# Optimization experiments

Measured on AMD Instinct MI355X. Metric: run time of the kernel, lower is better.

## Reference

```python
import jax, jax.numpy as jnp
import numpy as np

DIM = 192
HEADS = 6

def conv1x1(x, w):
    # x: [b,c,h,w], w: [out,in]
    return jnp.einsum('oi,bihw->bohw', w, x)

def dwconv3x3(x, w):
    # x: [b,c,h,w], w: [c,1,3,3] depthwise
    return jax.lax.conv_general_dilated(
        x, w, window_strides=(1, 1), padding='SAME',
        dimension_numbers=('NCHW', 'OIHW', 'NCHW'),
        feature_group_count=x.shape[1])

def l2norm(x, eps=1e-12):
    n = jnp.sqrt(jnp.sum(x * x, axis=-1, keepdims=True))
    return x / jnp.maximum(n, eps)

def setup_inputs() -> dict:
    key = jax.random.key(0)
    ks = jax.random.split(key, 9)
    b, c, h, w = 8, DIM, 128, 128
    s = 1.0 / np.sqrt(c)
    return {
        'x': jax.random.normal(ks[0], (b, c, h, w), jnp.float32),
        'Wq': jax.random.normal(ks[1], (c, c), jnp.float32) * s,
        'Wk': jax.random.normal(ks[2], (c, c), jnp.float32) * s,
        'Wv': jax.random.normal(ks[3], (c, c), jnp.float32) * s,
        'Wq_dw': jax.random.normal(ks[4], (c, 1, 3, 3), jnp.float32) * (1.0 / 3.0),
        'Wk_dw': jax.random.normal(ks[5], (c, 1, 3, 3), jnp.float32) * (1.0 / 3.0),
        'Wv_dw': jax.random.normal(ks[6], (c, 1, 3, 3), jnp.float32) * (1.0 / 3.0),
        'rescale': jnp.ones((HEADS, 1, 1), jnp.float32),
        'Wp': jax.random.normal(ks[7], (c, c), jnp.float32) * s,
    }

def reference(x, Wq, Wk, Wv, Wq_dw, Wk_dw, Wv_dw, rescale, Wp):
    b, c, h, w = x.shape
    hd = c // HEADS  # per-head channels
    q = dwconv3x3(conv1x1(x, Wq), Wq_dw).reshape(b, HEADS, hd, h * w)
    k = dwconv3x3(conv1x1(x, Wk), Wk_dw).reshape(b, HEADS, hd, h * w)
    v = dwconv3x3(conv1x1(x, Wv), Wv_dw).reshape(b, HEADS, hd, h * w)
    q = l2norm(q)
    k = l2norm(k)
    # attn: [b, heads, hd, hd] -- small channel-wise attention
    attn = jnp.einsum('bhcn,bhdn->bhcd', q, k) * rescale
    attn = jax.nn.softmax(attn, axis=-1)
    out = jnp.einsum('bhcd,bhdn->bhcn', attn, v).reshape(b, c, h, w)
    return conv1x1(out, Wp)
```

## Files before the change

### kernel.cpp

```cpp
#include <hip/hip_runtime.h>
#include <hip/hip_bf16.h>


using bf16x8 = __attribute__((ext_vector_type(8))) short;
using f32x4  = __attribute__((ext_vector_type(4))) float;
using fvec4  = __attribute__((ext_vector_type(4))) float;

#define NB     8
#define CDIM   192
#define NHEADS 6
#define IMGW   128
#define NPIX   16384

__device__ __forceinline__ float b2f(unsigned short u){
  return __uint_as_float(((unsigned int)u) << 16);
}
__device__ __forceinline__ unsigned short f2b(float f){
  unsigned int x = __float_as_uint(f);
  return (unsigned short)((x + 0x7FFFu + ((x >> 16) & 1u)) >> 16);
}
__device__ __forceinline__ float ldT(const void* p, size_t i, int isbf){
  return isbf ? b2f(((const unsigned short*)p)[i]) : ((const float*)p)[i];
}
__device__ __forceinline__ f32x4 MF(bf16x8 a, bf16x8 b, f32x4 c){
  return __builtin_amdgcn_mfma_f32_16x16x32_bf16(a, b, c, 0, 0, 0);
}

__global__ void k_detect(const unsigned short* x, int* flag){
  int l = threadIdx.x;
  int cnt = 0;
#pragma unroll
  for (int i = 0; i < 2; ++i){
    unsigned short u = x[(l*2 + i)*2];
    float a = fabsf(b2f(u));
    if (a == 0.f || (a > 1e-4f && a < 20.f)) ++cnt;
  }
  int tot = __popcll(__ballot(cnt >= 1)) + __popcll(__ballot(cnt >= 2));
  if (l == 0) *flag = (tot > 64) ? 1 : 0;
}

__global__ __launch_bounds__(256) void k_prep(const void* Wq, const void* Wk, const void* Wv,
    unsigned short* Wqkv, const int* flag){
  int i = blockIdx.x*256 + threadIdx.x;
  if (i >= 576*192) return;
  int isbf = *flag;
  int m = i / 192, kk = i % 192;
  int t = m / 192;
  const void* W = (t == 0) ? Wq : (t == 1) ? Wk : Wv;
  Wqkv[i] = f2b(ldT(W, (size_t)(m % 192)*192 + kk, isbf));
}

__global__ __launch_bounds__(256) void k_conv1(const void* x, const unsigned short* Wqkv,
    unsigned short* q0, unsigned short* k0, unsigned short* v0, const int* flag){
  __shared__ unsigned short Bt[64][200];
  __shared__ unsigned short outb[192][72];
  int tid = threadIdx.x;
  int ntr = blockIdx.x, b = blockIdx.y;
  int nt = (ntr & 7)*32 + (ntr >> 3);
  int n0 = nt * 64;
  int isbf = *flag;
  if (isbf){
    const unsigned short* xs = (const unsigned short*)x;
    for (int r = tid; r < 1536; r += 256){
      int k = r >> 3, j8 = (r & 7) * 8;
      int s = (r & 7) << 3;
      bf16x8 v = *(const bf16x8*)(xs + (size_t)(b*CDIM + k)*NPIX + n0 + j8);
      int kx = k ^ s;
#pragma unroll
      for (int i = 0; i < 8; ++i) Bt[j8+i][kx] = (unsigned short)v[i];
    }
  } else {
    const float* xf = (const float*)x;
    for (int r = tid; r < 3072; r += 256){
      int k = r >> 4, j4 = (r & 15) * 4;
      int s = ((j4 >> 3) & 7) << 3;
      fvec4 v = *(const fvec4*)(xf + (size_t)(b*CDIM + k)*NPIX + n0 + j4);
      int kx = k ^ s;
#pragma unroll
      for (int i = 0; i < 4; ++i) Bt[j4+i][kx] = f2b(v[i]);
    }
  }
  __syncthreads();
  int w = tid >> 6, l = tid & 63, lr = l & 15, lk = l >> 4;
#pragma unroll 1
  for (int t = 0; t < 3; ++t){
    f32x4 acc[3][4] = {};
    for (int kc = 0; kc < 6; ++kc){
      bf16x8 af[3];
#pragma unroll
      for (int g = 0; g < 3; ++g)
        af[g] = *(const bf16x8*)(Wqkv + ((size_t)t*CDIM + g*64 + w*16 + lr)*CDIM + kc*32 + lk*8);
#pragma unroll
      for (int nf = 0; nf < 4; ++nf){
        int nrow = nf*16 + lr;
        int s = ((nrow >> 3) & 7) << 3;
        bf16x8 bfv = *(const bf16x8*)(&Bt[nrow][(kc*32 + lk*8) ^ s]);
#pragma unroll
        for (int g = 0; g < 3; ++g) acc[g][nf] = MF(af[g], bfv, acc[g][nf]);
      }
    }
    __syncthreads();
#pragma unroll
    for (int g = 0; g < 3; ++g)
#pragma unroll
      for (int nf = 0; nf < 4; ++nf)
#pragma unroll
        for (int r = 0; r < 4; ++r)
          outb[g*64 + w*16 + lk*4 + r][nf*16 + lr] = f2b(acc[g][nf][r]);
    __syncthreads();
    unsigned short* dst = ((t == 0) ? q0 : (t == 1) ? k0 : v0) + (size_t)b*CDIM*NPIX;
    for (int e = tid; e < 1536; e += 256){
      int m = e >> 3, p8 = (e & 7) * 8;
      *(bf16x8*)(dst + (size_t)m*NPIX + n0 + p8) = *(const bf16x8*)(&outb[m][p8]);
    }
  }
}

__global__ __launch_bounds__(256) void k_dw(unsigned short* q0, unsigned short* k0,
    unsigned short* v0, const void* wqd, const void* wkd, const void* wvd,
    float* Nsq, const int* flag){
  __shared__ unsigned short img[128][136];
  __shared__ unsigned short outb[128][136];
  __shared__ float wred[4];
  int tid = threadIdx.x;
  int t = blockIdx.x, c = blockIdx.y, b = blockIdx.z;
  int isbf = *flag;
  unsigned short* base = ((t == 0) ? q0 : (t == 1) ? k0 : v0) + (size_t)(b*CDIM + c)*NPIX;
  const void* wd = (t == 0) ? wqd : (t == 1) ? wkd : wvd;
  float w9[9];
#pragma unroll
  for (int e = 0; e < 9; ++e) w9[e] = ldT(wd, (size_t)c*9 + e, isbf);
  for (int r = tid; r < 2048; r += 256){
    int row = r >> 4, col8 = (r & 15)*8;
    *(bf16x8*)(&img[row][col8]) = *(const bf16x8*)(base + row*IMGW + col8);
  }
  __syncthreads();
  int tr = tid >> 2, tc = tid & 3;
  int c0 = tc * 32, r0 = tr * 2;
  const bf16x8 zv = {0,0,0,0,0,0,0,0};
  int  rowi[4]; bool valid[4];
  bf16x8 cur[4], nxt[4];
  float carry[4];
#pragma unroll
  for (int d = 0; d < 4; ++d){
    rowi[d] = r0 - 1 + d;
    valid[d] = (rowi[d] >= 0) && (rowi[d] < 128);
    cur[d] = valid[d] ? *(const bf16x8*)(&img[rowi[d]][c0]) : zv;
    carry[d] = (valid[d] && c0 > 0) ? b2f(img[rowi[d]][c0 - 1]) : 0.f;
  }
  float sq = 0.f;
#pragma unroll
  for (int j = 0; j < 4; ++j){
    float right0[4];
    if (j < 3){
#pragma unroll
      for (int d = 0; d < 4; ++d){
        nxt[d] = valid[d] ? *(const bf16x8*)(&img[rowi[d]][c0 + 8*(j+1)]) : zv;
        right0[d] = b2f((unsigned short)nxt[d][0]);
      }
    } else {
#pragma unroll
      for (int d = 0; d < 4; ++d)
        right0[d] = (valid[d] && (c0 + 32 < 128)) ? b2f(img[rowi[d]][c0 + 32]) : 0.f;
    }
    float f[4][8];
#pragma unroll
    for (int d = 0; d < 4; ++d)
#pragma unroll
      for (int i = 0; i < 8; ++i) f[d][i] = b2f((unsigned short)cur[d][i]);
#pragma unroll
    for (int rr = 0; rr < 2; ++rr){
      float o[8];
#pragma unroll
      for (int cc = 0; cc < 8; ++cc){
        float a = 0.f;
#pragma unroll
        for (int d2 = 0; d2 < 3; ++d2){
          int d = rr + d2;
          float lf = (cc == 0) ? carry[d] : f[d][cc-1];
          float md = f[d][cc];
          float rt = (cc == 7) ? right0[d] : f[d][cc+1];
          a = fmaf(w9[d2*3+0], lf, a);
          a = fmaf(w9[d2*3+1], md, a);
          a = fmaf(w9[d2*3+2], rt, a);
        }
        o[cc] = a;
        if (t < 2) sq = fmaf(a, a, sq);
      }
      bf16x8 ov;
#pragma unroll
      for (int cc = 0; cc < 8; ++cc) ov[cc] = (short)f2b(o[cc]);
      *(bf16x8*)(&outb[r0 + rr][c0 + 8*j]) = ov;
    }
#pragma unroll
    for (int d = 0; d < 4; ++d) carry[d] = f[d][7];
    if (j < 3){
#pragma unroll
      for (int d = 0; d < 4; ++d) cur[d] = nxt[d];
    }
  }
  if (t < 2){
#pragma unroll
    for (int off = 32; off > 0; off >>= 1) sq += __shfl_xor(sq, off);
    if ((tid & 63) == 0) wred[tid >> 6] = sq;
  }
  __syncthreads();
  for (int e = tid; e < 2048; e += 256){
    int row = e >> 4, p8 = (e & 15) * 8;
    *(bf16x8*)(base + row*IMGW + p8) = *(const bf16x8*)(&outb[row][p8]);
  }
  if (t < 2 && tid == 0)
    Nsq[((size_t)b*2 + t)*CDIM + c] = wred[0] + wred[1] + wred[2] + wred[3];
}

__global__ __launch_bounds__(256) void k_gram(const unsigned short* qd,
    const unsigned short* kd, float* Spart){
  __shared__ float S_lds[1024];
  int tid = threadIdx.x;
  int cs = blockIdx.x, h = blockIdx.y, b = blockIdx.z;
  int w = tid >> 6, l = tid & 63, lr = l & 15, lk = l >> 4;
  for (int e = tid; e < 1024; e += 256) S_lds[e] = 0.f;
  __syncthreads();
  const unsigned short* qb = qd + (size_t)(b*CDIM + h*32)*NPIX;
  const unsigned short* kb = kd + (size_t)(b*CDIM + h*32)*NPIX;
  f32x4 g4[2][2] = {};
  int pxb = cs*2048 + w*512 + lk*8;
#pragma unroll
  for (int kc = 0; kc < 16; ++kc){
    int px = pxb + kc*32;
    bf16x8 a0 = *(const bf16x8*)(qb + (size_t)lr*NPIX + px);
    bf16x8 a1 = *(const bf16x8*)(qb + (size_t)(16+lr)*NPIX + px);
    bf16x8 b0 = *(const bf16x8*)(kb + (size_t)lr*NPIX + px);
    bf16x8 b1 = *(const bf16x8*)(kb + (size_t)(16+lr)*NPIX + px);
    g4[0][0] = MF(a0, b0, g4[0][0]);
    g4[0][1] = MF(a0, b1, g4[0][1]);
    g4[1][0] = MF(a1, b0, g4[1][0]);
    g4[1][1] = MF(a1, b1, g4[1][1]);
  }
  for (int wv = 0; wv < 4; ++wv){
    if (w == wv){
#pragma unroll
      for (int mi = 0; mi < 2; ++mi)
#pragma unroll
        for (int ni = 0; ni < 2; ++ni)
#pragma unroll
          for (int r = 0; r < 4; ++r)
            S_lds[(mi*16 + lk*4 + r)*32 + ni*16 + lr] += g4[mi][ni][r];
    }
    __syncthreads();
  }
  int bidx = (b*NHEADS + h)*8 + cs;
  for (int e = tid; e < 1024; e += 256) Spart[(size_t)bidx*1024 + e] = S_lds[e];
}

__global__ __launch_bounds__(256) void k_attn(const float* Spart, const float* Nsq,
    const void* rescale, float* attnG, const int* flag){
  __shared__ float S[1024];
  __shared__ float rn[64];
  int bh = blockIdx.x, tid = threadIdx.x;
  int b = bh / NHEADS, h = bh % NHEADS;
  int isbf = *flag;
  for (int e = tid; e < 1024; e += 256){
    float a = 0.f;
    for (int st = 0; st < 8; ++st) a += Spart[((size_t)bh*8 + st)*1024 + e];
    S[e] = a;
  }
  if (tid < 64){
    int t = tid >> 5, ch = h*32 + (tid & 31);
    float a = Nsq[((size_t)b*2 + t)*CDIM + ch];
    rn[tid] = 1.f / fmaxf(sqrtf(a), 1e-12f);
  }
  __syncthreads();
  if (tid < 32){
    float sc = ldT(rescale, h, isbf);
    float lo[32], mx = -1e30f;
#pragma unroll
    for (int d = 0; d < 32; ++d){
      lo[d] = S[tid*32 + d] * rn[tid] * rn[32 + d] * sc;
      mx = fmaxf(mx, lo[d]);
    }
    float sum = 0.f;
#pragma unroll
    for (int d = 0; d < 32; ++d){ lo[d] = __expf(lo[d] - mx); sum += lo[d]; }
    float inv = 1.f / sum;
#pragma unroll
    for (int d = 0; d < 32; ++d) attnG[(size_t)bh*1024 + tid*32 + d] = lo[d] * inv;
  }
}

__global__ __launch_bounds__(256) void k_mmat(const void* Wp, const float* attnG,
    unsigned short* Mb, const int* flag){
  __shared__ float at[NHEADS*1024];
  __shared__ float wp[32][200];
  int b = blockIdx.x, og = blockIdx.y, tid = threadIdx.x;
  int isbf = *flag;
  for (int e = tid; e < NHEADS*1024; e += 256) at[e] = attnG[(size_t)b*NHEADS*1024 + e];
  for (int e = tid; e < 32*192; e += 256){
    int r = e / 192, cdx = e % 192;
    wp[r][cdx] = ldT(Wp, (size_t)(og*32 + r)*CDIM + cdx, isbf);
  }
  __syncthreads();
  int r = tid >> 3, cg = tid & 7;
#pragma unroll 1
  for (int i = 0; i < 24; ++i){
    int dg = cg*24 + i;
    int hh = dg >> 5, d = dg & 31;
    float a = 0.f;
#pragma unroll
    for (int cc = 0; cc < 32; ++cc)
      a += wp[r][hh*32 + cc] * at[hh*1024 + cc*32 + d];
    Mb[(size_t)b*CDIM*CDIM + (size_t)(og*32 + r)*CDIM + dg] = f2b(a);
  }
}

__global__ __launch_bounds__(256) void k_out(const unsigned short* v, const unsigned short* Mb,
    void* out, const int* flag){
  __shared__ unsigned short Bt[64][200];
  __shared__ unsigned short outb[192][72];
  int tid = threadIdx.x;
  int ntr = blockIdx.x, b = blockIdx.y;
  int nt = (ntr & 7)*32 + (ntr >> 3);
  int n0 = nt * 64;
  for (int r = tid; r < 1536; r += 256){
    int k = r >> 3, j8 = (r & 7) * 8;
    int s = (r & 7) << 3;
    bf16x8 vv = *(const bf16x8*)(v + (size_t)(b*CDIM + k)*NPIX + n0 + j8);
    int kx = k ^ s;
#pragma unroll
    for (int i = 0; i < 8; ++i) Bt[j8+i][kx] = (unsigned short)vv[i];
  }
  __syncthreads();
  int w = tid >> 6, l = tid & 63, lr = l & 15, lk = l >> 4;
  const unsigned short* A = Mb + (size_t)b*CDIM*CDIM;
  f32x4 acc[3][4] = {};
  for (int kc = 0; kc < 6; ++kc){
    bf16x8 af[3];
#pragma unroll
    for (int g = 0; g < 3; ++g)
      af[g] = *(const bf16x8*)(A + (size_t)(g*64 + w*16 + lr)*CDIM + kc*32 + lk*8);
#pragma unroll
    for (int nf = 0; nf < 4; ++nf){
      int nrow = nf*16 + lr;
      int s = ((nrow >> 3) & 7) << 3;
      bf16x8 bfv = *(const bf16x8*)(&Bt[nrow][(kc*32 + lk*8) ^ s]);
#pragma unroll
      for (int g = 0; g < 3; ++g) acc[g][nf] = MF(af[g], bfv, acc[g][nf]);
    }
  }
  int isbf = *flag;
  if (isbf){
#pragma unroll
    for (int g = 0; g < 3; ++g)
#pragma unroll
      for (int nf = 0; nf < 4; ++nf)
#pragma unroll
        for (int r = 0; r < 4; ++r)
          outb[g*64 + w*16 + lk*4 + r][nf*16 + lr] = f2b(acc[g][nf][r]);
    __syncthreads();
    unsigned short* dst = (unsigned short*)out + (size_t)b*CDIM*NPIX;
    for (int e = tid; e < 1536; e += 256){
      int m = e >> 3, p8 = (e & 7) * 8;
      *(bf16x8*)(dst + (size_t)m*NPIX + n0 + p8) = *(const bf16x8*)(&outb[m][p8]);
    }
  } else {
#pragma unroll
    for (int g = 0; g < 3; ++g)
#pragma unroll
      for (int nf = 0; nf < 4; ++nf)
#pragma unroll
        for (int r = 0; r < 4; ++r){
          int m = g*64 + w*16 + lk*4 + r;
          ((float*)out)[(size_t)(b*CDIM + m)*NPIX + n0 + nf*16 + lr] = acc[g][nf][r];
        }
  }
}

extern "C" void kernel_launch(void* const* d_in, const int* in_sizes, int n_in,
                              void* d_out, int out_size, void* d_ws, size_t ws_size,
                              hipStream_t stream){
  const void* x   = d_in[0];
  const void* Wq  = d_in[1];
  const void* Wk  = d_in[2];
  const void* Wv  = d_in[3];
  const void* Wqd = d_in[4];
  const void* Wkd = d_in[5];
  const void* Wvd = d_in[6];
  const void* rsc = d_in[7];
  const void* Wp  = d_in[8];

  char* ws = (char*)d_ws;
  size_t o = 0;
  int* flag             = (int*)(ws + o);            o += 256;
  unsigned short* Wqkv  = (unsigned short*)(ws + o); o += (size_t)576*192*2;
  unsigned short* q0    = (unsigned short*)(ws + o); o += (size_t)NB*CDIM*NPIX*2;
  unsigned short* k0    = (unsigned short*)(ws + o); o += (size_t)NB*CDIM*NPIX*2;
  unsigned short* v0    = (unsigned short*)(ws + o); o += (size_t)NB*CDIM*NPIX*2;
  float* Spart          = (float*)(ws + o);          o += (size_t)384*1024*4;
  float* Nsq            = (float*)(ws + o);          o += (size_t)NB*2*CDIM*4;
  float* attnG          = (float*)(ws + o);          o += (size_t)48*1024*4;
  unsigned short* Mb    = (unsigned short*)(ws + o); o += (size_t)NB*CDIM*CDIM*2;

  k_detect<<<dim3(1), 64, 0, stream>>>((const unsigned short*)x, flag);
  k_prep  <<<dim3(432), 256, 0, stream>>>(Wq, Wk, Wv, Wqkv, flag);
  k_conv1 <<<dim3(256, NB), 256, 0, stream>>>(x, Wqkv, q0, k0, v0, flag);
  k_dw    <<<dim3(3, CDIM, NB), 256, 0, stream>>>(q0, k0, v0, Wqd, Wkd, Wvd, Nsq, flag);
  k_gram  <<<dim3(8, NHEADS, NB), 256, 0, stream>>>(q0, k0, Spart);
  k_attn  <<<dim3(48), 256, 0, stream>>>(Spart, Nsq, rsc, attnG, flag);
  k_mmat  <<<dim3(NB, 6), 256, 0, stream>>>(Wp, attnG, Mb, flag);
  k_out   <<<dim3(256, NB), 256, 0, stream>>>(v0, Mb, d_out, flag);
}
```

Before: 260.7 us.

## Fuse depthwise conv with Gram computation and store conv1 output in tiled layout

Merges the depthwise 3x3 conv and the q·k Gram kernel into one kernel. Each block processes 8 image rows for one head, keeps the convolved q and k rows in LDS, and computes partial Gram and norm sums there, so the q/k round trip through global memory goes away. Conv1 output is now written in a per-64-pixel tile layout [b][tile][c][64], and the convolved v goes to a separate buffer in the same layout that k_out reads. The cost is heavy LDS use (about 160KB, one block per CU), row-by-row syncs, and twice as many partial sums to reduce in k_attn.

```diff
diff --git a/kernel.cpp b/kernel.cpp
--- a/kernel.cpp
+++ b/kernel.cpp
@@ -11,6 +11,7 @@
 #define NHEADS 6
 #define IMGW   128
 #define NPIX   16384
+#define DDP    1032
 
 __device__ __forceinline__ float b2f(unsigned short u){
   return __uint_as_float(((unsigned int)u) << 16);
@@ -108,130 +109,122 @@
         for (int r = 0; r < 4; ++r)
           outb[g*64 + w*16 + lk*4 + r][nf*16 + lr] = f2b(acc[g][nf][r]);
     __syncthreads();
-    unsigned short* dst = ((t == 0) ? q0 : (t == 1) ? k0 : v0) + (size_t)b*CDIM*NPIX;
+    unsigned short* dstT = ((t == 0) ? q0 : (t == 1) ? k0 : v0)
+                         + (size_t)(b*256 + nt)*CDIM*64;
     for (int e = tid; e < 1536; e += 256){
       int m = e >> 3, p8 = (e & 7) * 8;
-      *(bf16x8*)(dst + (size_t)m*NPIX + n0 + p8) = *(const bf16x8*)(&outb[m][p8]);
-    }
-  }
-}
-
-__global__ __launch_bounds__(256) void k_dw(unsigned short* q0, unsigned short* k0,
-    unsigned short* v0, const void* wqd, const void* wkd, const void* wvd,
-    float* Nsq, const int* flag){
-  __shared__ unsigned short img[128][136];
-  __shared__ unsigned short outb[128][136];
-  __shared__ float wred[4];
+      *(bf16x8*)(dstT + m*64 + p8) = *(const bf16x8*)(&outb[m][p8]);
+    }
+  }
+}
+
+__global__ __launch_bounds__(256, 1) void k_dwg(const unsigned short* q0,
+    const unsigned short* k0, const unsigned short* v0,
+    const void* wqd, const void* wkd, const void* wvd,
+    unsigned short* v1, float* Spart, float* Npart, const int* flag){
+  __shared__ unsigned short ring[3][32][136];
+  __shared__ unsigned short qd[32*DDP];
+  __shared__ unsigned short kd[32*DDP];
+  __shared__ float S_lds[1024];
+  __shared__ float nbuf[2][32];
   int tid = threadIdx.x;
-  int t = blockIdx.x, c = blockIdx.y, b = blockIdx.z;
-  int isbf = *flag;
-  unsigned short* base = ((t == 0) ? q0 : (t == 1) ? k0 : v0) + (size_t)(b*CDIM + c)*NPIX;
-  const void* wd = (t == 0) ? wqd : (t == 1) ? wkd : wvd;
-  float w9[9];
-#pragma unroll
-  for (int e = 0; e < 9; ++e) w9[e] = ldT(wd, (size_t)c*9 + e, isbf);
-  for (int r = tid; r < 2048; r += 256){
-    int row = r >> 4, col8 = (r & 15)*8;
-    *(bf16x8*)(&img[row][col8]) = *(const bf16x8*)(base + row*IMGW + col8);
+  int s = blockIdx.x, h = blockIdx.y, b = blockIdx.z;
+  int isbf = *flag;
+  int r0 = s*8;
+  for (int e = tid; e < 1024; e += 256) S_lds[e] = 0.f;
+  int ch = tid >> 3, p0 = (tid & 7) * 16;
+  int chg = h*32 + ch;
+  int sch0 = tid >> 4,      sseg0 = tid & 15;
+  int sch1 = (tid+256) >> 4, sseg1 = (tid+256) & 15;
+  const int order[3] = {2, 0, 1};
+#pragma unroll 1
+  for (int tt = 0; tt < 3; ++tt){
+    int t = order[tt];
+    const unsigned short* src = (t == 0) ? q0 : (t == 1) ? k0 : v0;
+    const void* wd = (t == 0) ? wqd : (t == 1) ? wkd : wvd;
+    unsigned short* dd = (t == 1) ? kd : qd;
+    float w9[9];
+#pragma unroll
+    for (int e = 0; e < 9; ++e) w9[e] = ldT(wd, (size_t)chg*9 + e, isbf);
+    const bf16x8 zv = {0,0,0,0,0,0,0,0};
+    auto gload = [&](int r, bf16x8& a, bf16x8& c){
+      if (r >= 0 && r < 128){
+        int t0 = 2*r + (sseg0 >> 3), t1 = 2*r + (sseg1 >> 3);
+        a = *(const bf16x8*)(src + ((size_t)(b*256 + t0)*CDIM + h*32 + sch0)*64 + (sseg0 & 7)*8);
+        c = *(const bf16x8*)(src + ((size_t)(b*256 + t1)*CDIM + h*32 + sch1)*64 + (sseg1 & 7)*8);
+      } else { a = zv; c = zv; }
+    };
+    auto dswr = [&](int r, bf16x8 a, bf16x8 c){
+      int sl = ((r % 3) + 3) % 3;
+      *(bf16x8*)(&ring[sl][sch0][sseg0*8]) = a;
+      *(bf16x8*)(&ring[sl][sch1][sseg1*8]) = c;
+    };
+    bf16x8 pa, pc;
+    gload(r0-1, pa, pc); dswr(r0-1, pa, pc);
+    gload(r0,   pa, pc); dswr(r0,   pa, pc);
+    gload(r0+1, pa, pc);
+    __syncthreads();
+    float sq = 0.f;
+#pragma unroll 1
+    for (int rr = 0; rr < 8; ++rr){
+      int r = r0 + rr;
+      dswr(r+1, pa, pc);
+      __syncthreads();
+      if (rr < 7) gload(r+2, pa, pc);
+      float f[3][18];
+#pragma unroll
+      for (int j = 0; j < 3; ++j){
+        int sl = (((r-1+j) % 3) + 3) % 3;
+        const unsigned short* rp = &ring[sl][ch][0];
+        bf16x8 m0 = *(const bf16x8*)(rp + p0);
+        bf16x8 m1 = *(const bf16x8*)(rp + p0 + 8);
+        f[j][0]  = (p0 > 0)   ? b2f(rp[p0-1])  : 0.f;
+        f[j][17] = (p0 < 112) ? b2f(rp[p0+16]) : 0.f;
+#pragma unroll
+        for (int i = 0; i < 8; ++i){ f[j][1+i] = b2f((unsigned short)m0[i]);
+                                     f[j][9+i] = b2f((unsigned short)m1[i]); }
+      }
+      bf16x8 o0, o1;
+#pragma unroll
+      for (int c = 0; c < 16; ++c){
+        float a = 0.f;
+#pragma unroll
+        for (int j = 0; j < 3; ++j)
+#pragma unroll
+          for (int d = 0; d < 3; ++d)
+            a = fmaf(w9[j*3+d], f[j][c+d], a);
+        if (t < 2) sq = fmaf(a, a, sq);
+        if (c < 8) o0[c] = (short)f2b(a); else o1[c-8] = (short)f2b(a);
+      }
+      *(bf16x8*)(&dd[ch*DDP + rr*128 + p0])     = o0;
+      *(bf16x8*)(&dd[ch*DDP + rr*128 + p0 + 8]) = o1;
+      __syncthreads();
+    }
+    if (t < 2){
+      sq += __shfl_xor(sq, 1); sq += __shfl_xor(sq, 2); sq += __shfl_xor(sq, 4);
+      if ((tid & 7) == 0) nbuf[t][ch] = sq;
+    } else {
+      __syncthreads();
+      for (int e = tid; e < 4096; e += 256){
+        int c = e >> 7, chunk = e & 127;
+        int rr2 = chunk >> 4, px = (chunk & 15) * 8;
+        int tile = 2*(r0 + rr2) + (px >> 6);
+        *(bf16x8*)(v1 + ((size_t)(b*256 + tile)*CDIM + h*32 + c)*64 + (px & 63))
+          = *(const bf16x8*)(&qd[c*DDP + rr2*128 + px]);
+      }
+      __syncthreads();
+    }
   }
   __syncthreads();
-  int tr = tid >> 2, tc = tid & 3;
-  int c0 = tc * 32, r0 = tr * 2;
-  const bf16x8 zv = {0,0,0,0,0,0,0,0};
-  int  rowi[4]; bool valid[4];
-  bf16x8 cur[4], nxt[4];
-  float carry[4];
-#pragma unroll
-  for (int d = 0; d < 4; ++d){
-    rowi[d] = r0 - 1 + d;
-    valid[d] = (rowi[d] >= 0) && (rowi[d] < 128);
-    cur[d] = valid[d] ? *(const bf16x8*)(&img[rowi[d]][c0]) : zv;
-    carry[d] = (valid[d] && c0 > 0) ? b2f(img[rowi[d]][c0 - 1]) : 0.f;
-  }
-  float sq = 0.f;
-#pragma unroll
-  for (int j = 0; j < 4; ++j){
-    float right0[4];
-    if (j < 3){
-#pragma unroll
-      for (int d = 0; d < 4; ++d){
-        nxt[d] = valid[d] ? *(const bf16x8*)(&img[rowi[d]][c0 + 8*(j+1)]) : zv;
-        right0[d] = b2f((unsigned short)nxt[d][0]);
-      }
-    } else {
-#pragma unroll
-      for (int d = 0; d < 4; ++d)
-        right0[d] = (valid[d] && (c0 + 32 < 128)) ? b2f(img[rowi[d]][c0 + 32]) : 0.f;
-    }
-    float f[4][8];
-#pragma unroll
-    for (int d = 0; d < 4; ++d)
-#pragma unroll
-      for (int i = 0; i < 8; ++i) f[d][i] = b2f((unsigned short)cur[d][i]);
-#pragma unroll
-    for (int rr = 0; rr < 2; ++rr){
-      float o[8];
-#pragma unroll
-      for (int cc = 0; cc < 8; ++cc){
-        float a = 0.f;
-#pragma unroll
-        for (int d2 = 0; d2 < 3; ++d2){
-          int d = rr + d2;
-          float lf = (cc == 0) ? carry[d] : f[d][cc-1];
-          float md = f[d][cc];
-          float rt = (cc == 7) ? right0[d] : f[d][cc+1];
-          a = fmaf(w9[d2*3+0], lf, a);
-          a = fmaf(w9[d2*3+1], md, a);
-          a = fmaf(w9[d2*3+2], rt, a);
-        }
-        o[cc] = a;
-        if (t < 2) sq = fmaf(a, a, sq);
-      }
-      bf16x8 ov;
-#pragma unroll
-      for (int cc = 0; cc < 8; ++cc) ov[cc] = (short)f2b(o[cc]);
-      *(bf16x8*)(&outb[r0 + rr][c0 + 8*j]) = ov;
-    }
-#pragma unroll
-    for (int d = 0; d < 4; ++d) carry[d] = f[d][7];
-    if (j < 3){
-#pragma unroll
-      for (int d = 0; d < 4; ++d) cur[d] = nxt[d];
-    }
-  }
-  if (t < 2){
-#pragma unroll
-    for (int off = 32; off > 0; off >>= 1) sq += __shfl_xor(sq, off);
-    if ((tid & 63) == 0) wred[tid >> 6] = sq;
-  }
-  __syncthreads();
-  for (int e = tid; e < 2048; e += 256){
-    int row = e >> 4, p8 = (e & 15) * 8;
-    *(bf16x8*)(base + row*IMGW + p8) = *(const bf16x8*)(&outb[row][p8]);
-  }
-  if (t < 2 && tid == 0)
-    Nsq[((size_t)b*2 + t)*CDIM + c] = wred[0] + wred[1] + wred[2] + wred[3];
-}
-
-__global__ __launch_bounds__(256) void k_gram(const unsigned short* qd,
-    const unsigned short* kd, float* Spart){
-  __shared__ float S_lds[1024];
-  int tid = threadIdx.x;
-  int cs = blockIdx.x, h = blockIdx.y, b = blockIdx.z;
   int w = tid >> 6, l = tid & 63, lr = l & 15, lk = l >> 4;
-  for (int e = tid; e < 1024; e += 256) S_lds[e] = 0.f;
-  __syncthreads();
-  const unsigned short* qb = qd + (size_t)(b*CDIM + h*32)*NPIX;
-  const unsigned short* kb = kd + (size_t)(b*CDIM + h*32)*NPIX;
   f32x4 g4[2][2] = {};
-  int pxb = cs*2048 + w*512 + lk*8;
-#pragma unroll
-  for (int kc = 0; kc < 16; ++kc){
-    int px = pxb + kc*32;
-    bf16x8 a0 = *(const bf16x8*)(qb + (size_t)lr*NPIX + px);
-    bf16x8 a1 = *(const bf16x8*)(qb + (size_t)(16+lr)*NPIX + px);
-    bf16x8 b0 = *(const bf16x8*)(kb + (size_t)lr*NPIX + px);
-    bf16x8 b1 = *(const bf16x8*)(kb + (size_t)(16+lr)*NPIX + px);
+#pragma unroll
+  for (int kc = 0; kc < 8; ++kc){
+    int px = w*256 + kc*32 + lk*8;
+    bf16x8 a0 = *(const bf16x8*)(&qd[lr*DDP + px]);
+    bf16x8 a1 = *(const bf16x8*)(&qd[(16+lr)*DDP + px]);
+    bf16x8 b0 = *(const bf16x8*)(&kd[lr*DDP + px]);
+    bf16x8 b1 = *(const bf16x8*)(&kd[(16+lr)*DDP + px]);
     g4[0][0] = MF(a0, b0, g4[0][0]);
     g4[0][1] = MF(a0, b1, g4[0][1]);
     g4[1][0] = MF(a1, b0, g4[1][0]);
@@ -249,11 +242,15 @@
     }
     __syncthreads();
   }
-  int bidx = (b*NHEADS + h)*8 + cs;
-  for (int e = tid; e < 1024; e += 256) Spart[(size_t)bidx*1024 + e] = S_lds[e];
-}
-
-__global__ __launch_bounds__(256) void k_attn(const float* Spart, const float* Nsq,
+  size_t bidx = ((size_t)(b*NHEADS + h)*16 + s);
+  for (int e = tid; e < 1024; e += 256) Spart[bidx*1024 + e] = S_lds[e];
+  if (tid < 64){
+    int tq = tid >> 5, c32 = tid & 31;
+    Npart[((((size_t)b*2 + tq)*NHEADS + h)*32 + c32)*16 + s] = nbuf[tq][c32];
+  }
+}
+
+__global__ __launch_bounds__(256) void k_attn(const float* Spart, const float* Npart,
     const void* rescale, float* attnG, const int* flag){
   __shared__ float S[1024];
   __shared__ float rn[64];
@@ -262,12 +259,14 @@
   int isbf = *flag;
   for (int e = tid; e < 1024; e += 256){
     float a = 0.f;
-    for (int st = 0; st < 8; ++st) a += Spart[((size_t)bh*8 + st)*1024 + e];
+    for (int st = 0; st < 16; ++st) a += Spart[((size_t)bh*16 + st)*1024 + e];
     S[e] = a;
   }
   if (tid < 64){
-    int t = tid >> 5, ch = h*32 + (tid & 31);
-    float a = Nsq[((size_t)b*2 + t)*CDIM + ch];
+    int t = tid >> 5, c32 = tid & 31;
+    float a = 0.f;
+    for (int st = 0; st < 16; ++st)
+      a += Npart[((((size_t)b*2 + t)*NHEADS + h)*32 + c32)*16 + st];
     rn[tid] = 1.f / fmaxf(sqrtf(a), 1e-12f);
   }
   __syncthreads();
@@ -321,10 +320,11 @@
   int ntr = blockIdx.x, b = blockIdx.y;
   int nt = (ntr & 7)*32 + (ntr >> 3);
   int n0 = nt * 64;
+  const unsigned short* vtile = v + (size_t)(b*256 + nt)*CDIM*64;
   for (int r = tid; r < 1536; r += 256){
     int k = r >> 3, j8 = (r & 7) * 8;
     int s = (r & 7) << 3;
-    bf16x8 vv = *(const bf16x8*)(v + (size_t)(b*CDIM + k)*NPIX + n0 + j8);
+    bf16x8 vv = *(const bf16x8*)(vtile + (size_t)k*64 + j8);
     int kx = k ^ s;
 #pragma unroll
     for (int i = 0; i < 8; ++i) Bt[j8+i][kx] = (unsigned short)vv[i];
@@ -395,17 +395,18 @@
   unsigned short* q0    = (unsigned short*)(ws + o); o += (size_t)NB*CDIM*NPIX*2;
   unsigned short* k0    = (unsigned short*)(ws + o); o += (size_t)NB*CDIM*NPIX*2;
   unsigned short* v0    = (unsigned short*)(ws + o); o += (size_t)NB*CDIM*NPIX*2;
-  float* Spart          = (float*)(ws + o);          o += (size_t)384*1024*4;
-  float* Nsq            = (float*)(ws + o);          o += (size_t)NB*2*CDIM*4;
+  unsigned short* v1    = (unsigned short*)(ws + o); o += (size_t)NB*CDIM*NPIX*2;
+  float* Spart          = (float*)(ws + o);          o += (size_t)768*1024*4;
+  float* Npart          = (float*)(ws + o);          o += (size_t)NB*2*NHEADS*32*16*4;
   float* attnG          = (float*)(ws + o);          o += (size_t)48*1024*4;
   unsigned short* Mb    = (unsigned short*)(ws + o); o += (size_t)NB*CDIM*CDIM*2;
 
   k_detect<<<dim3(1), 64, 0, stream>>>((const unsigned short*)x, flag);
   k_prep  <<<dim3(432), 256, 0, stream>>>(Wq, Wk, Wv, Wqkv, flag);
   k_conv1 <<<dim3(256, NB), 256, 0, stream>>>(x, Wqkv, q0, k0, v0, flag);
-  k_dw    <<<dim3(3, CDIM, NB), 256, 0, stream>>>(q0, k0, v0, Wqd, Wkd, Wvd, Nsq, flag);
-  k_gram  <<<dim3(8, NHEADS, NB), 256, 0, stream>>>(q0, k0, Spart);
-  k_attn  <<<dim3(48), 256, 0, stream>>>(Spart, Nsq, rsc, attnG, flag);
+  k_dwg   <<<dim3(16, NHEADS, NB), 256, 0, stream>>>(q0, k0, v0, Wqd, Wkd, Wvd,
+                                                     v1, Spart, Npart, flag);
+  k_attn  <<<dim3(48), 256, 0, stream>>>(Spart, Npart, rsc, attnG, flag);
   k_mmat  <<<dim3(NB, 6), 256, 0, stream>>>(Wp, attnG, Mb, flag);
-  k_out   <<<dim3(256, NB), 256, 0, stream>>>(v0, Mb, d_out, flag);
-}
+  k_out   <<<dim3(256, NB), 256, 0, stream>>>(v1, Mb, d_out, flag);
+}
```

Result: slower. 280.9 us (+7.8%).

## Tile q/k/v intermediates per pixel block, shrink LDS, prefetch weight fragments

Applied to the files above, without the earlier changes.

The q/k/v intermediate buffers change from channel-major planes to per-64-pixel-tile blocks of 192x64, so the conv1 and out kernels read and write each tile as one contiguous block. The dwconv and gram kernels are re-indexed to this tiled layout. The conv1 and out kernels also shrink their output staging LDS to 64 rows, writing in three passes with extra barriers. They add launch_bounds occupancy hints and register double-buffering of the weight fragments across k-chunks. In exchange, dwconv and gram now issue more scattered strided accesses (rows split across tiles spaced TP apart), and the extra syncs add overhead.

```diff
diff --git a/kernel.cpp b/kernel.cpp
--- a/kernel.cpp
+++ b/kernel.cpp
@@ -11,6 +11,7 @@
 #define NHEADS 6
 #define IMGW   128
 #define NPIX   16384
+#define TP     12288
 
 __device__ __forceinline__ float b2f(unsigned short u){
   return __uint_as_float(((unsigned int)u) << 16);
@@ -50,10 +51,10 @@
   Wqkv[i] = f2b(ldT(W, (size_t)(m % 192)*192 + kk, isbf));
 }
 
-__global__ __launch_bounds__(256) void k_conv1(const void* x, const unsigned short* Wqkv,
+__global__ __launch_bounds__(256, 4) void k_conv1(const void* x, const unsigned short* Wqkv,
     unsigned short* q0, unsigned short* k0, unsigned short* v0, const int* flag){
   __shared__ unsigned short Bt[64][200];
-  __shared__ unsigned short outb[192][72];
+  __shared__ unsigned short outb[64][72];
   int tid = threadIdx.x;
   int ntr = blockIdx.x, b = blockIdx.y;
   int nt = (ntr & 7)*32 + (ntr >> 3);
@@ -85,33 +86,43 @@
 #pragma unroll 1
   for (int t = 0; t < 3; ++t){
     f32x4 acc[3][4] = {};
+    bf16x8 afc[3], afn[3];
+#pragma unroll
+    for (int g = 0; g < 3; ++g)
+      afc[g] = *(const bf16x8*)(Wqkv + ((size_t)t*CDIM + g*64 + w*16 + lr)*CDIM + lk*8);
+#pragma unroll 1
     for (int kc = 0; kc < 6; ++kc){
-      bf16x8 af[3];
-#pragma unroll
-      for (int g = 0; g < 3; ++g)
-        af[g] = *(const bf16x8*)(Wqkv + ((size_t)t*CDIM + g*64 + w*16 + lr)*CDIM + kc*32 + lk*8);
+      if (kc < 5){
+#pragma unroll
+        for (int g = 0; g < 3; ++g)
+          afn[g] = *(const bf16x8*)(Wqkv + ((size_t)t*CDIM + g*64 + w*16 + lr)*CDIM + (kc+1)*32 + lk*8);
+      }
 #pragma unroll
       for (int nf = 0; nf < 4; ++nf){
         int nrow = nf*16 + lr;
         int s = ((nrow >> 3) & 7) << 3;
         bf16x8 bfv = *(const bf16x8*)(&Bt[nrow][(kc*32 + lk*8) ^ s]);
 #pragma unroll
-        for (int g = 0; g < 3; ++g) acc[g][nf] = MF(af[g], bfv, acc[g][nf]);
-      }
-    }
-    __syncthreads();
-#pragma unroll
-    for (int g = 0; g < 3; ++g)
+        for (int g = 0; g < 3; ++g) acc[g][nf] = MF(afc[g], bfv, acc[g][nf]);
+      }
+#pragma unroll
+      for (int g = 0; g < 3; ++g) afc[g] = afn[g];
+    }
+    unsigned short* dstT = ((t == 0) ? q0 : (t == 1) ? k0 : v0)
+                         + (size_t)(b*256 + nt)*TP;
+#pragma unroll 1
+    for (int g = 0; g < 3; ++g){
+      __syncthreads();
 #pragma unroll
       for (int nf = 0; nf < 4; ++nf)
 #pragma unroll
         for (int r = 0; r < 4; ++r)
-          outb[g*64 + w*16 + lk*4 + r][nf*16 + lr] = f2b(acc[g][nf][r]);
-    __syncthreads();
-    unsigned short* dst = ((t == 0) ? q0 : (t == 1) ? k0 : v0) + (size_t)b*CDIM*NPIX;
-    for (int e = tid; e < 1536; e += 256){
-      int m = e >> 3, p8 = (e & 7) * 8;
-      *(bf16x8*)(dst + (size_t)m*NPIX + n0 + p8) = *(const bf16x8*)(&outb[m][p8]);
+          outb[w*16 + lk*4 + r][nf*16 + lr] = f2b(acc[g][nf][r]);
+      __syncthreads();
+      for (int e = tid; e < 512; e += 256){
+        int m64 = e >> 3, p8 = (e & 7) * 8;
+        *(bf16x8*)(dstT + (g*64 + m64)*64 + p8) = *(const bf16x8*)(&outb[m64][p8]);
+      }
     }
   }
 }
@@ -125,14 +136,16 @@
   int tid = threadIdx.x;
   int t = blockIdx.x, c = blockIdx.y, b = blockIdx.z;
   int isbf = *flag;
-  unsigned short* base = ((t == 0) ? q0 : (t == 1) ? k0 : v0) + (size_t)(b*CDIM + c)*NPIX;
+  unsigned short* base = ((t == 0) ? q0 : (t == 1) ? k0 : v0)
+                       + (size_t)(b*256)*TP + c*64;
   const void* wd = (t == 0) ? wqd : (t == 1) ? wkd : wvd;
   float w9[9];
 #pragma unroll
   for (int e = 0; e < 9; ++e) w9[e] = ldT(wd, (size_t)c*9 + e, isbf);
   for (int r = tid; r < 2048; r += 256){
     int row = r >> 4, col8 = (r & 15)*8;
-    *(bf16x8*)(&img[row][col8]) = *(const bf16x8*)(base + row*IMGW + col8);
+    *(bf16x8*)(&img[row][col8]) =
+      *(const bf16x8*)(base + (size_t)(2*row + (col8 >> 6))*TP + (col8 & 63));
   }
   __syncthreads();
   int tr = tid >> 2, tc = tid & 3;
@@ -207,7 +220,8 @@
   __syncthreads();
   for (int e = tid; e < 2048; e += 256){
     int row = e >> 4, p8 = (e & 15) * 8;
-    *(bf16x8*)(base + row*IMGW + p8) = *(const bf16x8*)(&outb[row][p8]);
+    *(bf16x8*)(base + (size_t)(2*row + (p8 >> 6))*TP + (p8 & 63))
+      = *(const bf16x8*)(&outb[row][p8]);
   }
   if (t < 2 && tid == 0)
     Nsq[((size_t)b*2 + t)*CDIM + c] = wred[0] + wred[1] + wred[2] + wred[3];
@@ -221,17 +235,18 @@
   int w = tid >> 6, l = tid & 63, lr = l & 15, lk = l >> 4;
   for (int e = tid; e < 1024; e += 256) S_lds[e] = 0.f;
   __syncthreads();
-  const unsigned short* qb = qd + (size_t)(b*CDIM + h*32)*NPIX;
-  const unsigned short* kb = kd + (size_t)(b*CDIM + h*32)*NPIX;
+  const unsigned short* qb = qd + (size_t)(b*256)*TP + (h*32)*64;
+  const unsigned short* kb = kd + (size_t)(b*256)*TP + (h*32)*64;
   f32x4 g4[2][2] = {};
   int pxb = cs*2048 + w*512 + lk*8;
 #pragma unroll
   for (int kc = 0; kc < 16; ++kc){
     int px = pxb + kc*32;
-    bf16x8 a0 = *(const bf16x8*)(qb + (size_t)lr*NPIX + px);
-    bf16x8 a1 = *(const bf16x8*)(qb + (size_t)(16+lr)*NPIX + px);
-    bf16x8 b0 = *(const bf16x8*)(kb + (size_t)lr*NPIX + px);
-    bf16x8 b1 = *(const bf16x8*)(kb + (size_t)(16+lr)*NPIX + px);
+    size_t toff = (size_t)(px >> 6)*TP + (px & 63);
+    bf16x8 a0 = *(const bf16x8*)(qb + toff + lr*64);
+    bf16x8 a1 = *(const bf16x8*)(qb + toff + (16+lr)*64);
+    bf16x8 b0 = *(const bf16x8*)(kb + toff + lr*64);
+    bf16x8 b1 = *(const bf16x8*)(kb + toff + (16+lr)*64);
     g4[0][0] = MF(a0, b0, g4[0][0]);
     g4[0][1] = MF(a0, b1, g4[0][1]);
     g4[1][0] = MF(a1, b0, g4[1][0]);
@@ -313,18 +328,19 @@
   }
 }
 
-__global__ __launch_bounds__(256) void k_out(const unsigned short* v, const unsigned short* Mb,
+__global__ __launch_bounds__(256, 4) void k_out(const unsigned short* v, const unsigned short* Mb,
     void* out, const int* flag){
   __shared__ unsigned short Bt[64][200];
-  __shared__ unsigned short outb[192][72];
+  __shared__ unsigned short outb[64][72];
   int tid = threadIdx.x;
   int ntr = blockIdx.x, b = blockIdx.y;
   int nt = (ntr & 7)*32 + (ntr >> 3);
   int n0 = nt * 64;
+  const unsigned short* vtile = v + (size_t)(b*256 + nt)*TP;
   for (int r = tid; r < 1536; r += 256){
     int k = r >> 3, j8 = (r & 7) * 8;
     int s = (r & 7) << 3;
-    bf16x8 vv = *(const bf16x8*)(v + (size_t)(b*CDIM + k)*NPIX + n0 + j8);
+    bf16x8 vv = *(const bf16x8*)(vtile + (size_t)k*64 + j8);
     int kx = k ^ s;
 #pragma unroll
     for (int i = 0; i < 8; ++i) Bt[j8+i][kx] = (unsigned short)vv[i];
@@ -333,34 +349,45 @@
   int w = tid >> 6, l = tid & 63, lr = l & 15, lk = l >> 4;
   const unsigned short* A = Mb + (size_t)b*CDIM*CDIM;
   f32x4 acc[3][4] = {};
+  bf16x8 afc[3], afn[3];
+#pragma unroll
+  for (int g = 0; g < 3; ++g)
+    afc[g] = *(const bf16x8*)(A + (size_t)(g*64 + w*16 + lr)*CDIM + lk*8);
+#pragma unroll 1
   for (int kc = 0; kc < 6; ++kc){
-    bf16x8 af[3];
-#pragma unroll
-    for (int g = 0; g < 3; ++g)
-      af[g] = *(const bf16x8*)(A + (size_t)(g*64 + w*16 + lr)*CDIM + kc*32 + lk*8);
+    if (kc < 5){
+#pragma unroll
+      for (int g = 0; g < 3; ++g)
+        afn[g] = *(const bf16x8*)(A + (size_t)(g*64 + w*16 + lr)*CDIM + (kc+1)*32 + lk*8);
+    }
 #pragma unroll
     for (int nf = 0; nf < 4; ++nf){
       int nrow = nf*16 + lr;
       int s = ((nrow >> 3) & 7) << 3;
       bf16x8 bfv = *(const bf16x8*)(&Bt[nrow][(kc*32 + lk*8) ^ s]);
 #pragma unroll
-      for (int g = 0; g < 3; ++g) acc[g][nf] = MF(af[g], bfv, acc[g][nf]);
-    }
+      for (int g = 0; g < 3; ++g) acc[g][nf] = MF(afc[g], bfv, acc[g][nf]);
+    }
+#pragma unroll
+    for (int g = 0; g < 3; ++g) afc[g] = afn[g];
   }
   int isbf = *flag;
   if (isbf){
-#pragma unroll
-    for (int g = 0; g < 3; ++g)
+    unsigned short* dst = (unsigned short*)out + (size_t)b*CDIM*NPIX;
+#pragma unroll 1
+    for (int g = 0; g < 3; ++g){
+      __syncthreads();
 #pragma unroll
       for (int nf = 0; nf < 4; ++nf)
 #pragma unroll
         for (int r = 0; r < 4; ++r)
-          outb[g*64 + w*16 + lk*4 + r][nf*16 + lr] = f2b(acc[g][nf][r]);
-    __syncthreads();
-    unsigned short* dst = (unsigned short*)out + (size_t)b*CDIM*NPIX;
-    for (int e = tid; e < 1536; e += 256){
-      int m = e >> 3, p8 = (e & 7) * 8;
-      *(bf16x8*)(dst + (size_t)m*NPIX + n0 + p8) = *(const bf16x8*)(&outb[m][p8]);
+          outb[w*16 + lk*4 + r][nf*16 + lr] = f2b(acc[g][nf][r]);
+      __syncthreads();
+      for (int e = tid; e < 512; e += 256){
+        int m64 = e >> 3, p8 = (e & 7) * 8;
+        *(bf16x8*)(dst + (size_t)(g*64 + m64)*NPIX + n0 + p8)
+          = *(const bf16x8*)(&outb[m64][p8]);
+      }
     }
   } else {
 #pragma unroll
```

New measurement: 371.6 us. 1.43x slower.

## Fuse V depthwise conv into output GEMM kernel, drop V pass from k_dw

Applied to the files above, without the earlier changes.

The depthwise 3x3 convolution on V is moved out of k_dw, which now handles only q and k, and is computed on the fly inside k_out while its GEMM B tile is staged into LDS. This removes one full read and write pass over the V tensor in global memory and about a third of the k_dw blocks. In exchange k_out recomputes the stencil from global memory with neighbouring-row and edge-pixel loads, using a serial per-thread loop over 384 channel-half tasks spread across 256 threads, so load imbalance and scalar halo reads may lengthen the GEMM prologue.

```diff
diff --git a/kernel.cpp b/kernel.cpp
--- a/kernel.cpp
+++ b/kernel.cpp
@@ -117,16 +117,15 @@
 }
 
 __global__ __launch_bounds__(256) void k_dw(unsigned short* q0, unsigned short* k0,
-    unsigned short* v0, const void* wqd, const void* wkd, const void* wvd,
-    float* Nsq, const int* flag){
+    const void* wqd, const void* wkd, float* Nsq, const int* flag){
   __shared__ unsigned short img[128][136];
   __shared__ unsigned short outb[128][136];
   __shared__ float wred[4];
   int tid = threadIdx.x;
   int t = blockIdx.x, c = blockIdx.y, b = blockIdx.z;
   int isbf = *flag;
-  unsigned short* base = ((t == 0) ? q0 : (t == 1) ? k0 : v0) + (size_t)(b*CDIM + c)*NPIX;
-  const void* wd = (t == 0) ? wqd : (t == 1) ? wkd : wvd;
+  unsigned short* base = ((t == 0) ? q0 : k0) + (size_t)(b*CDIM + c)*NPIX;
+  const void* wd = (t == 0) ? wqd : wkd;
   float w9[9];
 #pragma unroll
   for (int e = 0; e < 9; ++e) w9[e] = ldT(wd, (size_t)c*9 + e, isbf);
@@ -185,7 +184,7 @@
           a = fmaf(w9[d2*3+2], rt, a);
         }
         o[cc] = a;
-        if (t < 2) sq = fmaf(a, a, sq);
+        sq = fmaf(a, a, sq);
       }
       bf16x8 ov;
 #pragma unroll
@@ -199,17 +198,15 @@
       for (int d = 0; d < 4; ++d) cur[d] = nxt[d];
     }
   }
-  if (t < 2){
-#pragma unroll
-    for (int off = 32; off > 0; off >>= 1) sq += __shfl_xor(sq, off);
-    if ((tid & 63) == 0) wred[tid >> 6] = sq;
-  }
+#pragma unroll
+  for (int off = 32; off > 0; off >>= 1) sq += __shfl_xor(sq, off);
+  if ((tid & 63) == 0) wred[tid >> 6] = sq;
   __syncthreads();
   for (int e = tid; e < 2048; e += 256){
     int row = e >> 4, p8 = (e & 15) * 8;
     *(bf16x8*)(base + row*IMGW + p8) = *(const bf16x8*)(&outb[row][p8]);
   }
-  if (t < 2 && tid == 0)
+  if (tid == 0)
     Nsq[((size_t)b*2 + t)*CDIM + c] = wred[0] + wred[1] + wred[2] + wred[3];
 }
 
@@ -314,20 +311,52 @@
 }
 
 __global__ __launch_bounds__(256) void k_out(const unsigned short* v, const unsigned short* Mb,
-    void* out, const int* flag){
+    const void* wvd, void* out, const int* flag){
   __shared__ unsigned short Bt[64][200];
   __shared__ unsigned short outb[192][72];
   int tid = threadIdx.x;
   int ntr = blockIdx.x, b = blockIdx.y;
   int nt = (ntr & 7)*32 + (ntr >> 3);
   int n0 = nt * 64;
-  for (int r = tid; r < 1536; r += 256){
-    int k = r >> 3, j8 = (r & 7) * 8;
-    int s = (r & 7) << 3;
-    bf16x8 vv = *(const bf16x8*)(v + (size_t)(b*CDIM + k)*NPIX + n0 + j8);
-    int kx = k ^ s;
-#pragma unroll
-    for (int i = 0; i < 8; ++i) Bt[j8+i][kx] = (unsigned short)vv[i];
+  int row = n0 >> 7;
+  int isbf = *flag;
+  for (int e = tid; e < 384; e += 256){
+    int c = e >> 1, half = e & 1;
+    int p0 = (n0 & 127) + half*32;
+    float w9[9];
+#pragma unroll
+    for (int q = 0; q < 9; ++q) w9[q] = ldT(wvd, (size_t)c*9 + q, isbf);
+    const unsigned short* vb = v + (size_t)(b*CDIM + c)*NPIX + row*IMGW;
+#pragma unroll 1
+    for (int jc = 0; jc < 4; ++jc){
+      int c0 = p0 + jc*8;
+      float o[8] = {0.f,0.f,0.f,0.f,0.f,0.f,0.f,0.f};
+#pragma unroll
+      for (int dr = 0; dr < 3; ++dr){
+        int rr = row - 1 + dr;
+        if (rr >= 0 && rr < 128){
+          const unsigned short* rp = vb + (dr-1)*IMGW;
+          bf16x8 bv = *(const bf16x8*)(rp + c0);
+          float fl[10];
+          fl[0] = (c0 > 0)       ? b2f(rp[c0-1]) : 0.f;
+#pragma unroll
+          for (int i = 0; i < 8; ++i) fl[1+i] = b2f((unsigned short)bv[i]);
+          fl[9] = (c0 + 8 < 128) ? b2f(rp[c0+8]) : 0.f;
+#pragma unroll
+          for (int d = 0; d < 3; ++d){
+            float wv = w9[dr*3+d];
+#pragma unroll
+            for (int i = 0; i < 8; ++i) o[i] = fmaf(wv, fl[i+d], o[i]);
+          }
+        }
+      }
+#pragma unroll
+      for (int i = 0; i < 8; ++i){
+        int px = half*32 + jc*8 + i;
+        int s = ((px >> 3) & 7) << 3;
+        Bt[px][c ^ s] = f2b(o[i]);
+      }
+    }
   }
   __syncthreads();
   int w = tid >> 6, l = tid & 63, lr = l & 15, lk = l >> 4;
@@ -347,8 +376,8 @@
       for (int g = 0; g < 3; ++g) acc[g][nf] = MF(af[g], bfv, acc[g][nf]);
     }
   }
-  int isbf = *flag;
-  if (isbf){
+  int isbf2 = *flag;
+  if (isbf2){
 #pragma unroll
     for (int g = 0; g < 3; ++g)
 #pragma unroll
@@ -403,9 +432,9 @@
   k_detect<<<dim3(1), 64, 0, stream>>>((const unsigned short*)x, flag);
   k_prep  <<<dim3(432), 256, 0, stream>>>(Wq, Wk, Wv, Wqkv, flag);
   k_conv1 <<<dim3(256, NB), 256, 0, stream>>>(x, Wqkv, q0, k0, v0, flag);
-  k_dw    <<<dim3(3, CDIM, NB), 256, 0, stream>>>(q0, k0, v0, Wqd, Wkd, Wvd, Nsq, flag);
+  k_dw    <<<dim3(2, CDIM, NB), 256, 0, stream>>>(q0, k0, Wqd, Wkd, Nsq, flag);
   k_gram  <<<dim3(8, NHEADS, NB), 256, 0, stream>>>(q0, k0, Spart);
   k_attn  <<<dim3(48), 256, 0, stream>>>(Spart, Nsq, rsc, attnG, flag);
   k_mmat  <<<dim3(NB, 6), 256, 0, stream>>>(Wp, attnG, Mb, flag);
-  k_out   <<<dim3(256, NB), 256, 0, stream>>>(v0, Mb, d_out, flag);
-}
+  k_out   <<<dim3(256, NB), 256, 0, stream>>>(v0, Mb, Wvd, d_out, flag);
+}
```

Result: slower. 290.0 us (+11.2%).
